# Kernel tuning notes

Measured on AMD Instinct MI355X. Metric: run time of the kernel, lower is better.

The kernel has to match this reference:

```python
import jax, jax.numpy as jnp
import numpy as np
import math

B, T, M, C, H = 4, 1024, 256, 512, 8
HD = C // H
NEG = -1e30


def setup_inputs() -> dict:
    key = jax.random.key(0)
    ks = jax.random.split(key, 16)
    s = 1.0 / math.sqrt(C)
    inp = {
        'x': jax.random.normal(ks[0], (B, T, C), jnp.float32),
        'y': jax.random.normal(ks[1], (B, M, C), jnp.float32),
        'attn_x_mask': jnp.tril(jnp.ones((T, T), bool))[None, None],  # causal (1,1,T,T)
        'Wqkv_x': jax.random.normal(ks[2], (C, 3 * C), jnp.float32) * s,
        'bqkv_x': jnp.zeros((3 * C,), jnp.float32),
        'Wqkv_y': jax.random.normal(ks[3], (C, 3 * C), jnp.float32) * s,
        'bqkv_y': jnp.zeros((3 * C,), jnp.float32),
        'w4x': jax.random.normal(ks[4], (H, HD), jnp.float32) * math.sqrt(1.0 / C / 3),
        'w4y': jax.random.normal(ks[5], (H, HD), jnp.float32) * math.sqrt(1.0 / C / 3),
        'w4xy': jax.random.normal(ks[6], (H, HD), jnp.float32) * math.sqrt(1.0 / C / 3),
        'Wgs': jax.random.normal(ks[7], (C, C), jnp.float32) * s,
        'bgs': jnp.zeros((C,), jnp.float32),
        'Wgc': jax.random.normal(ks[8], (C, C), jnp.float32) * s,
        'bgc': jnp.zeros((C,), jnp.float32),
        'Wp': jax.random.normal(ks[9], (C, C), jnp.float32) * s,
        'bp': jnp.zeros((C,), jnp.float32),
    }
    return inp


def _heads(t):
    b, n, c = t.shape
    return t.reshape(b, n, H, HD).transpose(0, 2, 1, 3)  # (B,H,N,HD)


def reference(x, y, attn_x_mask, Wqkv_x, bqkv_x, Wqkv_y, bqkv_y,
              w4x, w4y, w4xy, Wgs, bgs, Wgc, bgc, Wp, bp):
    q_x, k_x, v_x = [_heads(t) for t in jnp.split(x @ Wqkv_x + bqkv_x, 3, axis=-1)]
    q_y, k_y, v_y = [_heads(t) for t in jnp.split(y @ Wqkv_y + bqkv_y, 3, axis=-1)]
    scale = 1.0 / math.sqrt(HD)

    # additive bias attention: catt1 (per query-x), catt2 (per key-y), catt3 (bilinear)
    catt1 = jnp.einsum('bhtd,hd->bht', q_x, w4x)[..., :, None]          # (B,H,T,1)
    catt2 = jnp.einsum('bhmd,hd->bhm', q_y, w4y)[:, :, None, :]          # (B,H,1,M)
    catt3 = jnp.einsum('bhtd,bhmd->bhtm', q_x * w4xy[None, :, None, :], k_y) * scale
    catt = catt1 + catt2 + catt3                                         # (B,H,T,M)

    catt_x2y = jax.nn.softmax(catt, axis=-1)
    catt_y2x = jax.nn.softmax(catt, axis=-2)

    cval_x2y = jnp.einsum('bhtm,bhmd->bhtd', catt_x2y, v_y)
    cval_x2y = cval_x2y.transpose(0, 2, 1, 3).reshape(B, T, C)

    # product-of-attentions: (T,M) @ (M,T) -> (T,T)
    chain = jnp.einsum('bhtm,bhsm->bhts', catt_x2y, catt_y2x) * (1.0 / math.sqrt(M))
    chain = jnp.where(attn_x_mask, chain, NEG)
    chain = jax.nn.softmax(chain, axis=-1)
    cval_y2x = jnp.einsum('bhts,bhsd->bhtd', chain, v_x)
    cval_y2x = cval_y2x.transpose(0, 2, 1, 3).reshape(B, T, C)

    cval = cval_x2y + cval_y2x + x

    # masked self-attention
    satt = jnp.einsum('bhtd,bhsd->bhts', q_x, k_x) * scale
    satt = jnp.where(attn_x_mask, satt, NEG)
    satt = jax.nn.softmax(satt, axis=-1)
    sval = jnp.einsum('bhts,bhsd->bhtd', satt, v_x).transpose(0, 2, 1, 3).reshape(B, T, C)

    sgate = jax.nn.sigmoid(sval @ Wgs + bgs)
    cgate = jax.nn.sigmoid(cval @ Wgc + bgc)
    out = (sgate * cval + cgate * sval) @ Wp + bp
    return out
```

## Files before the change

kernel.cpp:

```cpp
#include <hip/hip_runtime.h>
#include <hip/hip_bf16.h>

typedef __hip_bfloat16 bf16;
using f4 = __attribute__((ext_vector_type(4))) float;
using s8 = __attribute__((ext_vector_type(8))) short;
using s4 = __attribute__((ext_vector_type(4))) short;

__device__ __forceinline__ void storeOut(float* p, float v) { *p = v; }
__device__ __forceinline__ void storeOut(bf16* p, float v) { *p = __float2bfloat16(v); }
__device__ __forceinline__ short bfs(float x) { return __builtin_bit_cast(short, __float2bfloat16(x)); }

constexpr int B_ = 4, T_ = 1024, M_ = 256, C_ = 512, H_ = 8, HD_ = 64, C3_ = 1536;

#define MFMA16(a, b, c) __builtin_amdgcn_mfma_f32_16x16x32_bf16((a), (b), (c), 0, 0, 0)

__global__ __launch_bounds__(256) void prep_kernel(
    const float* __restrict__ Wqkv_x, const float* __restrict__ Wqkv_y,
    const float* __restrict__ Wgs, const float* __restrict__ Wgc, const float* __restrict__ Wp,
    const float* __restrict__ x, const float* __restrict__ y,
    bf16* __restrict__ WT_x, bf16* __restrict__ WT_y, bf16* __restrict__ WT_gs,
    bf16* __restrict__ WT_gc, bf16* __restrict__ WT_p,
    bf16* __restrict__ x_bf, bf16* __restrict__ y_bf)
{
    __shared__ float Ls[64][65];
    const int tid = threadIdx.x;
    const int bid = blockIdx.x;
    if (bid < 576) {
        const float* W; bf16* WT; int N, t;
        if (bid < 192)      { W = Wqkv_x; WT = WT_x;  N = C3_; t = bid; }
        else if (bid < 384) { W = Wqkv_y; WT = WT_y;  N = C3_; t = bid - 192; }
        else if (bid < 448) { W = Wgs;    WT = WT_gs; N = C_;  t = bid - 384; }
        else if (bid < 512) { W = Wgc;    WT = WT_gc; N = C_;  t = bid - 448; }
        else                { W = Wp;     WT = WT_p;  N = C_;  t = bid - 512; }
        const int K = C_;
        const int tw = N >> 6;
        const int n0 = (t % tw) * 64, k0 = (t / tw) * 64;
        for (int i = tid; i < 1024; i += 256) {
            int kr = i >> 4, ng = i & 15;
            float4 v = *(const float4*)&W[(size_t)(k0 + kr) * N + n0 + ng * 4];
            Ls[ng * 4 + 0][kr] = v.x; Ls[ng * 4 + 1][kr] = v.y;
            Ls[ng * 4 + 2][kr] = v.z; Ls[ng * 4 + 3][kr] = v.w;
        }
        __syncthreads();
        for (int i = tid; i < 512; i += 256) {
            int n = i >> 3, kg = i & 7;
            s8 r;
            #pragma unroll
            for (int j = 0; j < 8; ++j) r[j] = bfs(Ls[n][kg * 8 + j]);
            *(s8*)&WT[(size_t)(n0 + n) * K + k0 + kg * 8] = r;
        }
    } else if (bid < 1600) {
        int i = (bid - 576) * 2048 + tid * 8;
        s8 r;
        #pragma unroll
        for (int j = 0; j < 8; ++j) r[j] = bfs(x[i + j]);
        *(s8*)&x_bf[i] = r;
    } else {
        int i = (bid - 1600) * 2048 + tid * 8;
        s8 r;
        #pragma unroll
        for (int j = 0; j < 8; ++j) r[j] = bfs(y[i + j]);
        *(s8*)&y_bf[i] = r;
    }
}

__global__ __launch_bounds__(256) void qwcatt_kernel(
    const bf16* __restrict__ qkv_x, const bf16* __restrict__ qkv_y,
    const float* __restrict__ w4x, const float* __restrict__ w4y,
    float* __restrict__ catt1b, float* __restrict__ catt2b)
{
    int i = blockIdx.x * 256 + threadIdx.x;
    const bf16* row; const float* w; float* out; int oi;
    if (i < 32768) {
        int bh = i >> 10, t = i & 1023, b = bh >> 3, h = bh & 7;
        row = qkv_x + (size_t)(b * T_ + t) * C3_ + h * HD_;
        w = w4x + h * HD_; out = catt1b; oi = i;
    } else {
        int j = i - 32768;
        int bh = j >> 8, m = j & 255, b = bh >> 3, h = bh & 7;
        row = qkv_y + (size_t)(b * M_ + m) * C3_ + h * HD_;
        w = w4y + h * HD_; out = catt2b; oi = j;
    }
    float s = 0.f;
    #pragma unroll
    for (int d = 0; d < HD_; ++d) s = fmaf(__bfloat162float(row[d]), w[d], s);
    out[oi] = s;
}

template <typename OT>
__global__ __launch_bounds__(256) void gemm_staged_kernel(
    const bf16* __restrict__ A, const bf16* __restrict__ WT, const float* __restrict__ bias,
    OT* __restrict__ Cmat, int N, int K)
{
    __shared__ short Asb[128][72];
    __shared__ short Bsb[64][72];
    const int tid = threadIdx.x;
    const int wave = tid >> 6, lane = tid & 63;
    const int quad = lane >> 4, l16 = lane & 15;
    const int n0 = blockIdx.y * 64, m0 = blockIdx.x * 128;
    f4 acc[2][4];
    #pragma unroll
    for (int mt = 0; mt < 2; ++mt)
        #pragma unroll
        for (int nt = 0; nt < 4; ++nt) acc[mt][nt] = (f4)0.f;

    for (int k0 = 0; k0 < K; k0 += 64) {
        #pragma unroll
        for (int tl = 0; tl < 4; ++tl) {
            int g = tid + tl * 256, row = g >> 3, grp = g & 7;
            *(s8*)&Asb[row][grp * 8] = *(const s8*)&A[(size_t)(m0 + row) * K + k0 + grp * 8];
        }
        #pragma unroll
        for (int tl = 0; tl < 2; ++tl) {
            int g = tid + tl * 256, n = g >> 3, grp = g & 7;
            *(s8*)&Bsb[n][grp * 8] = *(const s8*)&WT[(size_t)(n0 + n) * K + k0 + grp * 8];
        }
        __syncthreads();
        #pragma unroll
        for (int ks = 0; ks < 2; ++ks) {
            s8 a0 = *(const s8*)&Asb[wave * 32 + l16][ks * 32 + quad * 8];
            s8 a1 = *(const s8*)&Asb[wave * 32 + 16 + l16][ks * 32 + quad * 8];
            #pragma unroll
            for (int nt = 0; nt < 4; ++nt) {
                s8 bv = *(const s8*)&Bsb[nt * 16 + l16][ks * 32 + quad * 8];
                acc[0][nt] = MFMA16(a0, bv, acc[0][nt]);
                acc[1][nt] = MFMA16(a1, bv, acc[1][nt]);
            }
        }
        __syncthreads();
    }
    #pragma unroll
    for (int mt = 0; mt < 2; ++mt)
        #pragma unroll
        for (int nt = 0; nt < 4; ++nt) {
            int col = n0 + nt * 16 + l16;
            float bb = bias[col];
            #pragma unroll
            for (int reg = 0; reg < 4; ++reg) {
                int row = m0 + wave * 32 + mt * 16 + quad * 4 + reg;
                storeOut(&Cmat[(size_t)row * N + col], acc[mt][nt][reg] + bb);
            }
        }
}

__global__ __launch_bounds__(256) void catt3r_kernel(
    const bf16* __restrict__ qkv_x, const bf16* __restrict__ qkv_y,
    const float* __restrict__ catt1, const float* __restrict__ catt2,
    const float* __restrict__ w4xy,
    bf16* __restrict__ x2y, float* __restrict__ rowsum_, float* __restrict__ psum)
{
    __shared__ float redc[4][256];
    const int tid = threadIdx.x;
    const int wave = tid >> 6, lane = tid & 63;
    const int quad = lane >> 4, l16 = lane & 15;
    const int bh = blockIdx.x, b = bh >> 3, h = bh & 7;
    const int t0 = blockIdx.y * 64;
    f4 sc[4][4];
    #pragma unroll
    for (int mt = 0; mt < 4; ++mt)
        #pragma unroll
        for (int nt = 0; nt < 4; ++nt) sc[mt][nt] = (f4)0.f;

    const bf16* ap = qkv_x + (size_t)(b * T_ + t0 + wave * 16 + l16) * C3_ + h * HD_ + quad * 8;
    s8 a0r = *(const s8*)ap;
    s8 a1r = *(const s8*)(ap + 32);
    const float* wx = w4xy + h * HD_ + quad * 8;
    s8 a0, a1;
    #pragma unroll
    for (int j = 0; j < 8; ++j) {
        a0[j] = bfs(__bfloat162float(__builtin_bit_cast(bf16, a0r[j])) * wx[j]);
        a1[j] = bfs(__bfloat162float(__builtin_bit_cast(bf16, a1r[j])) * wx[j + 32]);
    }
    const bf16* bp = qkv_y + (size_t)(b * M_ + l16) * C3_ + C_ + h * HD_ + quad * 8;
    #pragma unroll
    for (int mt = 0; mt < 4; ++mt)
        #pragma unroll
        for (int nt = 0; nt < 4; ++nt) {
            const bf16* bq = bp + (size_t)(mt * 64 + nt * 16) * C3_;
            sc[mt][nt] = MFMA16(a0, *(const s8*)bq, sc[mt][nt]);
            sc[mt][nt] = MFMA16(a1, *(const s8*)(bq + 32), sc[mt][nt]);
        }

    float c1[4];
    #pragma unroll
    for (int reg = 0; reg < 4; ++reg)
        c1[reg] = catt1[bh * T_ + t0 + wave * 16 + quad * 4 + reg];
    #pragma unroll
    for (int mt = 0; mt < 4; ++mt)
        #pragma unroll
        for (int nt = 0; nt < 4; ++nt) {
            float c2 = catt2[bh * M_ + mt * 64 + nt * 16 + l16];
            #pragma unroll
            for (int reg = 0; reg < 4; ++reg)
                sc[mt][nt][reg] = __expf(sc[mt][nt][reg] * 0.125f + c1[reg] + c2);
        }

    #pragma unroll
    for (int reg = 0; reg < 4; ++reg) {
        float rs = 0.f;
        #pragma unroll
        for (int mt = 0; mt < 4; ++mt)
            #pragma unroll
            for (int nt = 0; nt < 4; ++nt) rs += sc[mt][nt][reg];
        rs += __shfl_xor(rs, 1); rs += __shfl_xor(rs, 2);
        rs += __shfl_xor(rs, 4); rs += __shfl_xor(rs, 8);
        const int t = t0 + wave * 16 + quad * 4 + reg;
        if (l16 == 0) rowsum_[bh * T_ + t] = rs;
        const float ri = 1.f / rs;
        #pragma unroll
        for (int mt = 0; mt < 4; ++mt)
            #pragma unroll
            for (int nt = 0; nt < 4; ++nt)
                x2y[((size_t)bh * T_ + t) * M_ + mt * 64 + nt * 16 + l16] =
                    __float2bfloat16(sc[mt][nt][reg] * ri);
    }

    #pragma unroll
    for (int mt = 0; mt < 4; ++mt)
        #pragma unroll
        for (int nt = 0; nt < 4; ++nt) {
            float es = sc[mt][nt][0] + sc[mt][nt][1] + sc[mt][nt][2] + sc[mt][nt][3];
            es += __shfl_xor(es, 16);
            es += __shfl_xor(es, 32);
            if (quad == 0) redc[wave][mt * 64 + nt * 16 + l16] = es;
        }
    __syncthreads();
    psum[((size_t)bh * 16 + blockIdx.y) * M_ + tid] =
        redc[0][tid] + redc[1][tid] + redc[2][tid] + redc[3][tid];
}

__global__ __launch_bounds__(256) void colfin_vtrans_kernel(
    const float* __restrict__ psum, float* __restrict__ colinv,
    const bf16* __restrict__ qkv_x, const bf16* __restrict__ qkv_y,
    bf16* __restrict__ vTx, bf16* __restrict__ vTy)
{
    __shared__ short Ls[64][68];
    const int tid = threadIdx.x;
    int bid = blockIdx.x;
    if (bid < 32) {
        const int bh = bid, m = tid;
        float s = 0.f;
        #pragma unroll
        for (int ch = 0; ch < 16; ++ch) s += psum[(bh * 16 + ch) * M_ + m];
        colinv[bh * M_ + m] = 1.f / s;
        return;
    }
    bid -= 32;
    const bf16* qkv; bf16* vT; int Nrows, bh, t0;
    if (bid < 512) { qkv = qkv_x; vT = vTx; Nrows = T_; bh = bid >> 4; t0 = (bid & 15) * 64; }
    else { bid -= 512; qkv = qkv_y; vT = vTy; Nrows = M_; bh = bid >> 2; t0 = (bid & 3) * 64; }
    const int b = bh >> 3, h = bh & 7;
    for (int i = tid; i < 4096; i += 256) {
        int tl = i >> 6, d = i & 63;
        Ls[d][tl] = __builtin_bit_cast(short,
            qkv[(size_t)(b * Nrows + t0 + tl) * C3_ + 2 * C_ + h * HD_ + d]);
    }
    __syncthreads();
    for (int i = tid; i < 4096; i += 256) {
        int d = i >> 6, tl = i & 63;
        vT[((size_t)bh * 64 + d) * Nrows + t0 + tl] = __builtin_bit_cast(bf16, Ls[d][tl]);
    }
}

__global__ __launch_bounds__(512) void flash14_kernel(
    const bf16* __restrict__ x2y, const float* __restrict__ rowsum_,
    const float* __restrict__ colinv,
    const bf16* __restrict__ vTx, const bf16* __restrict__ vTy,
    const bf16* __restrict__ qkv_x, const float* __restrict__ x,
    bf16* __restrict__ cval_bf, bf16* __restrict__ sval_bf)
{
    __shared__ short Kc[64][264];
    __shared__ short Ksf[64][72];
    __shared__ short Vb[64][72];
    __shared__ short Ps[8][16][68];
    const int tid = threadIdx.x;
    const int wave = tid >> 6, lane = tid & 63;
    const int quad = lane >> 4, l16 = lane & 15;
    const int bh = blockIdx.x, b = bh >> 3, h = bh & 7;
    const int p = blockIdx.y;
    const int jt = (wave < 4) ? p : (15 - p);
    const int rb = jt * 64 + (wave & 3) * 16;
    const int nst = 16 - p;

    s8 qc[8], qs[2];
    {
        const bf16* qp = x2y + (size_t)(bh * T_ + rb + l16) * M_ + quad * 8;
        #pragma unroll
        for (int f = 0; f < 8; ++f) qc[f] = *(const s8*)(qp + f * 32);
        const bf16* qsp = qkv_x + (size_t)(b * T_ + rb + l16) * C3_ + h * HD_ + quad * 8;
        qs[0] = *(const s8*)qsp;
        qs[1] = *(const s8*)(qsp + 32);
    }

    f4 ocv[4];
    #pragma unroll
    for (int dt = 0; dt < 4; ++dt) ocv[dt] = (f4)0.f;
    {
        const bf16* vb = vTy + (size_t)(bh * 64 + l16) * M_ + quad * 8;
        #pragma unroll
        for (int f = 0; f < 8; ++f)
            #pragma unroll
            for (int dt = 0; dt < 4; ++dt) {
                s8 bv = *(const s8*)(vb + (size_t)dt * 16 * M_ + f * 32);
                ocv[dt] = MFMA16(qc[f], bv, ocv[dt]);
            }
    }

    #pragma unroll
    for (int f = 0; f < 8; ++f) {
        const float* cp = colinv + bh * M_ + f * 32 + quad * 8;
        s8 q = qc[f], r;
        #pragma unroll
        for (int j = 0; j < 8; ++j)
            r[j] = bfs(__bfloat162float(__builtin_bit_cast(bf16, q[j])) * cp[j]);
        qc[f] = r;
    }

    f4 oc[4], os_[4];
    float lc[4] = {0.f, 0.f, 0.f, 0.f}, ls_[4] = {0.f, 0.f, 0.f, 0.f};
    #pragma unroll
    for (int dt = 0; dt < 4; ++dt) { oc[dt] = (f4)0.f; os_[dt] = (f4)0.f; }

    #pragma unroll
    for (int tl = 0; tl < 4; ++tl) {
        int g = tid + tl * 512, row = g >> 5, grp = g & 31;
        *(s8*)&Kc[row][grp * 8] = *(const s8*)&x2y[(size_t)(bh * T_ + row) * M_ + grp * 8];
    }
    {
        int row = tid >> 3, grp = tid & 7;
        *(s8*)&Ksf[row][grp * 8] =
            *(const s8*)&qkv_x[(size_t)(b * T_ + row) * C3_ + C_ + h * HD_ + grp * 8];
        *(s8*)&Vb[row][grp * 8] = *(const s8*)&vTx[(size_t)(bh * 64 + row) * T_ + grp * 8];
    }
    __syncthreads();

    for (int st = 0; st < nst; ++st) {
        const int s0 = st * 64;
        const bool pf = (st + 1) < nst;
        s8 kcp[4], ksp, vp;
        if (pf) {
            const int sn = s0 + 64;
            #pragma unroll
            for (int tl = 0; tl < 4; ++tl) {
                int g = tid + tl * 512, row = g >> 5, grp = g & 31;
                kcp[tl] = *(const s8*)&x2y[(size_t)(bh * T_ + sn + row) * M_ + grp * 8];
            }
            int row = tid >> 3, grp = tid & 7;
            ksp = *(const s8*)&qkv_x[(size_t)(b * T_ + sn + row) * C3_ + C_ + h * HD_ + grp * 8];
            vp = *(const s8*)&vTx[(size_t)(bh * 64 + row) * T_ + sn + grp * 8];
        }
        if (st <= jt) {
            float rsS[4];
            #pragma unroll
            for (int nt = 0; nt < 4; ++nt)
                rsS[nt] = rowsum_[bh * T_ + s0 + nt * 16 + l16] * 0.0625f;
            f4 sc[4];
            #pragma unroll
            for (int nt = 0; nt < 4; ++nt) sc[nt] = (f4)0.f;
            #pragma unroll
            for (int f = 0; f < 8; ++f)
                #pragma unroll
                for (int nt = 0; nt < 4; ++nt) {
                    s8 bv = *(const s8*)&Kc[nt * 16 + l16][f * 32 + quad * 8];
                    sc[nt] = MFMA16(qc[f], bv, sc[nt]);
                }
            f4 ss[4];
            #pragma unroll
            for (int nt = 0; nt < 4; ++nt) ss[nt] = (f4)0.f;
            #pragma unroll
            for (int f = 0; f < 2; ++f)
                #pragma unroll
                for (int nt = 0; nt < 4; ++nt) {
                    s8 bv = *(const s8*)&Ksf[nt * 16 + l16][f * 32 + quad * 8];
                    ss[nt] = MFMA16(qs[f], bv, ss[nt]);
                }
            #pragma unroll
            for (int reg = 0; reg < 4; ++reg) {
                const int t_g = rb + quad * 4 + reg;
                #pragma unroll
                for (int nt = 0; nt < 4; ++nt) {
                    float pv = (s0 + nt * 16 + l16 <= t_g) ? __expf(sc[nt][reg] * rsS[nt]) : 0.f;
                    lc[reg] += pv;
                    Ps[wave][quad * 4 + reg][nt * 16 + l16] = bfs(pv);
                }
            }
            #pragma unroll
            for (int ks = 0; ks < 2; ++ks) {
                const short* pp = &Ps[wave][l16][ks * 32 + quad * 8];
                s4 alo = *(const s4*)pp;
                s4 ahi = *(const s4*)(pp + 4);
                s8 a;
                a[0] = alo[0]; a[1] = alo[1]; a[2] = alo[2]; a[3] = alo[3];
                a[4] = ahi[0]; a[5] = ahi[1]; a[6] = ahi[2]; a[7] = ahi[3];
                #pragma unroll
                for (int dt = 0; dt < 4; ++dt) {
                    s8 bv = *(const s8*)&Vb[dt * 16 + l16][ks * 32 + quad * 8];
                    oc[dt] = MFMA16(a, bv, oc[dt]);
                }
            }
            #pragma unroll
            for (int reg = 0; reg < 4; ++reg) {
                const int t_g = rb + quad * 4 + reg;
                #pragma unroll
                for (int nt = 0; nt < 4; ++nt) {
                    float pv = (s0 + nt * 16 + l16 <= t_g) ? __expf(ss[nt][reg] * 0.125f) : 0.f;
                    ls_[reg] += pv;
                    Ps[wave][quad * 4 + reg][nt * 16 + l16] = bfs(pv);
                }
            }
            #pragma unroll
            for (int ks = 0; ks < 2; ++ks) {
                const short* pp = &Ps[wave][l16][ks * 32 + quad * 8];
                s4 alo = *(const s4*)pp;
                s4 ahi = *(const s4*)(pp + 4);
                s8 a;
                a[0] = alo[0]; a[1] = alo[1]; a[2] = alo[2]; a[3] = alo[3];
                a[4] = ahi[0]; a[5] = ahi[1]; a[6] = ahi[2]; a[7] = ahi[3];
                #pragma unroll
                for (int dt = 0; dt < 4; ++dt) {
                    s8 bv = *(const s8*)&Vb[dt * 16 + l16][ks * 32 + quad * 8];
                    os_[dt] = MFMA16(a, bv, os_[dt]);
                }
            }
        }
        __syncthreads();
        if (pf) {
            #pragma unroll
            for (int tl = 0; tl < 4; ++tl) {
                int g = tid + tl * 512, row = g >> 5, grp = g & 31;
                *(s8*)&Kc[row][grp * 8] = kcp[tl];
            }
            int row = tid >> 3, grp = tid & 7;
            *(s8*)&Ksf[row][grp * 8] = ksp;
            *(s8*)&Vb[row][grp * 8] = vp;
        }
        __syncthreads();
    }

    #pragma unroll
    for (int reg = 0; reg < 4; ++reg) {
        float l1 = lc[reg], l2 = ls_[reg];
        l1 += __shfl_xor(l1, 1); l1 += __shfl_xor(l1, 2);
        l1 += __shfl_xor(l1, 4); l1 += __shfl_xor(l1, 8);
        l2 += __shfl_xor(l2, 1); l2 += __shfl_xor(l2, 2);
        l2 += __shfl_xor(l2, 4); l2 += __shfl_xor(l2, 8);
        const float i1 = 1.f / l1, i2 = 1.f / l2;
        const int t = rb + quad * 4 + reg;
        #pragma unroll
        for (int dt = 0; dt < 4; ++dt) {
            size_t idx = (size_t)(b * T_ + t) * C_ + h * HD_ + dt * 16 + l16;
            float cv = ocv[dt][reg] + oc[dt][reg] * i1 + x[idx];
            cval_bf[idx] = __float2bfloat16(cv);
            float sv = os_[dt][reg] * i2;
            sval_bf[idx] = __float2bfloat16(sv);
        }
    }
}

__global__ __launch_bounds__(256) void gatefuse_kernel(
    const bf16* __restrict__ svalb, const bf16* __restrict__ cvalb,
    const bf16* __restrict__ WTgs, const bf16* __restrict__ WTgc,
    const float* __restrict__ bgs, const float* __restrict__ bgc,
    bf16* __restrict__ gated)
{
    __shared__ short Sb[128][72], Cb[128][72], W1b[64][72], W2b[64][72];
    const int tid = threadIdx.x;
    const int wave = tid >> 6, lane = tid & 63;
    const int quad = lane >> 4, l16 = lane & 15;
    const int n0 = blockIdx.y * 64, m0 = blockIdx.x * 128;
    f4 aS[2][4], aC[2][4];
    #pragma unroll
    for (int mt = 0; mt < 2; ++mt)
        #pragma unroll
        for (int nt = 0; nt < 4; ++nt) { aS[mt][nt] = (f4)0.f; aC[mt][nt] = (f4)0.f; }

    for (int k0 = 0; k0 < C_; k0 += 64) {
        #pragma unroll
        for (int tl = 0; tl < 4; ++tl) {
            int g = tid + tl * 256, row = g >> 3, grp = g & 7;
            *(s8*)&Sb[row][grp * 8] = *(const s8*)&svalb[(size_t)(m0 + row) * C_ + k0 + grp * 8];
            *(s8*)&Cb[row][grp * 8] = *(const s8*)&cvalb[(size_t)(m0 + row) * C_ + k0 + grp * 8];
        }
        #pragma unroll
        for (int tl = 0; tl < 2; ++tl) {
            int g = tid + tl * 256, n = g >> 3, grp = g & 7;
            *(s8*)&W1b[n][grp * 8] = *(const s8*)&WTgs[(size_t)(n0 + n) * C_ + k0 + grp * 8];
            *(s8*)&W2b[n][grp * 8] = *(const s8*)&WTgc[(size_t)(n0 + n) * C_ + k0 + grp * 8];
        }
        __syncthreads();
        #pragma unroll
        for (int ks = 0; ks < 2; ++ks) {
            s8 s0f = *(const s8*)&Sb[wave * 32 + l16][ks * 32 + quad * 8];
            s8 s1f = *(const s8*)&Sb[wave * 32 + 16 + l16][ks * 32 + quad * 8];
            s8 c0f = *(const s8*)&Cb[wave * 32 + l16][ks * 32 + quad * 8];
            s8 c1f = *(const s8*)&Cb[wave * 32 + 16 + l16][ks * 32 + quad * 8];
            #pragma unroll
            for (int nt = 0; nt < 4; ++nt) {
                s8 w1 = *(const s8*)&W1b[nt * 16 + l16][ks * 32 + quad * 8];
                s8 w2 = *(const s8*)&W2b[nt * 16 + l16][ks * 32 + quad * 8];
                aS[0][nt] = MFMA16(s0f, w1, aS[0][nt]);
                aS[1][nt] = MFMA16(s1f, w1, aS[1][nt]);
                aC[0][nt] = MFMA16(c0f, w2, aC[0][nt]);
                aC[1][nt] = MFMA16(c1f, w2, aC[1][nt]);
            }
        }
        __syncthreads();
    }
    #pragma unroll
    for (int mt = 0; mt < 2; ++mt)
        #pragma unroll
        for (int nt = 0; nt < 4; ++nt) {
            int col = n0 + nt * 16 + l16;
            float b1 = bgs[col], b2 = bgc[col];
            #pragma unroll
            for (int reg = 0; reg < 4; ++reg) {
                int row = m0 + wave * 32 + mt * 16 + quad * 4 + reg;
                size_t idx = (size_t)row * C_ + col;
                float gs = 1.f / (1.f + __expf(-(aS[mt][nt][reg] + b1)));
                float gc = 1.f / (1.f + __expf(-(aC[mt][nt][reg] + b2)));
                float cvv = __bfloat162float(cvalb[idx]);
                float svv = __bfloat162float(svalb[idx]);
                gated[idx] = __float2bfloat16(gs * cvv + gc * svv);
            }
        }
}

extern "C" void kernel_launch(void* const* d_in, const int* in_sizes, int n_in,
                              void* d_out, int out_size, void* d_ws, size_t ws_size,
                              hipStream_t stream)
{
    const float* x      = (const float*)d_in[0];
    const float* y      = (const float*)d_in[1];
    const float* Wqkv_x = (const float*)d_in[3];
    const float* bqkv_x = (const float*)d_in[4];
    const float* Wqkv_y = (const float*)d_in[5];
    const float* bqkv_y = (const float*)d_in[6];
    const float* w4x    = (const float*)d_in[7];
    const float* w4y    = (const float*)d_in[8];
    const float* w4xy   = (const float*)d_in[9];
    const float* Wgs    = (const float*)d_in[10];
    const float* bgs    = (const float*)d_in[11];
    const float* Wgc    = (const float*)d_in[12];
    const float* bgc    = (const float*)d_in[13];
    const float* Wp     = (const float*)d_in[14];
    const float* bp     = (const float*)d_in[15];

    float* ws = (float*)d_ws;
    bf16*  qkv_x_bf = (bf16*)(ws + 0);
    bf16*  qkv_y_bf = (bf16*)(ws + 3145728);
    bf16*  gated_bf = (bf16*)(ws + 3932160);
    bf16*  cval_bf  = (bf16*)(ws + 5242880);
    bf16*  x2y_bf   = (bf16*)(ws + 12320768);
    bf16*  x_bf     = x2y_bf;
    bf16*  y_bf     = (bf16*)(ws + 13369344);
    bf16*  vTx_bf   = (bf16*)(ws + 20709376);
    bf16*  vTy_bf   = (bf16*)(ws + 21757952);
    float* psum_    = ws + 22020096;
    bf16*  qw_bf    = (bf16*)(ws + 26214400);
    bf16*  sval_bf  = qw_bf;
    bf16*  WT_x     = (bf16*)(ws + 27262976);
    bf16*  WT_y     = (bf16*)(ws + 27656192);
    bf16*  WT_gs    = (bf16*)(ws + 28049408);
    bf16*  WT_gc    = (bf16*)(ws + 28180480);
    bf16*  WT_p    = (bf16*)(ws + 28311552);
    float* catt1b   = ws + 28442624;
    float* catt2b   = ws + 28475392;
    float* colinv   = ws + 28483584;
    float* rowsum_  = ws + 28491776;

    prep_kernel<<<1856, 256, 0, stream>>>(
        Wqkv_x, Wqkv_y, Wgs, Wgc, Wp, x, y,
        WT_x, WT_y, WT_gs, WT_gc, WT_p, x_bf, y_bf);

    gemm_staged_kernel<bf16><<<dim3(32, 24), 256, 0, stream>>>(x_bf, WT_x, bqkv_x, qkv_x_bf, C3_, C_);
    gemm_staged_kernel<bf16><<<dim3(8, 24), 256, 0, stream>>>(y_bf, WT_y, bqkv_y, qkv_y_bf, C3_, C_);

    qwcatt_kernel<<<160, 256, 0, stream>>>(
        qkv_x_bf, qkv_y_bf, w4x, w4y, catt1b, catt2b);

    catt3r_kernel<<<dim3(32, 16), 256, 0, stream>>>(
        qkv_x_bf, qkv_y_bf, catt1b, catt2b, w4xy, x2y_bf, rowsum_, psum_);

    colfin_vtrans_kernel<<<672, 256, 0, stream>>>(psum_, colinv, qkv_x_bf, qkv_y_bf, vTx_bf, vTy_bf);

    flash14_kernel<<<dim3(32, 8), 512, 0, stream>>>(
        x2y_bf, rowsum_, colinv, vTx_bf, vTy_bf, qkv_x_bf, x, cval_bf, sval_bf);

    gatefuse_kernel<<<dim3(32, 8), 256, 0, stream>>>(
        sval_bf, cval_bf, WT_gs, WT_gc, bgs, bgc, gated_bf);

    gemm_staged_kernel<float><<<dim3(32, 8), 256, 0, stream>>>(
        gated_bf, WT_p, bp, (float*)d_out, C_, C_);
}
```

Measured before the change: 218.9 us.

## Merge QKV GEMMs, fuse catt1/2 with V transpose, fold column finalize into flash

The x and y QKV projections now run as one launch, with the block index selecting the operand set. The catt1/catt2 dot products are merged with the V-transpose kernel. The column-sum finalization (reciprocal of the summed partials) moves into the flash kernel, which reduces psum into shared memory, so the colfin step and its colinv buffer are gone. This cuts the pipeline from several small launches to fewer and removes their launch and tail overhead. In exchange, every flash block redundantly reads 16 partial sums per column.

```diff
diff --git a/kernel.cpp b/kernel.cpp
--- a/kernel.cpp
+++ b/kernel.cpp
@@ -64,27 +64,58 @@
     }
 }
 
-__global__ __launch_bounds__(256) void qwcatt_kernel(
-    const bf16* __restrict__ qkv_x, const bf16* __restrict__ qkv_y,
-    const float* __restrict__ w4x, const float* __restrict__ w4y,
-    float* __restrict__ catt1b, float* __restrict__ catt2b)
-{
-    int i = blockIdx.x * 256 + threadIdx.x;
-    const bf16* row; const float* w; float* out; int oi;
-    if (i < 32768) {
-        int bh = i >> 10, t = i & 1023, b = bh >> 3, h = bh & 7;
-        row = qkv_x + (size_t)(b * T_ + t) * C3_ + h * HD_;
-        w = w4x + h * HD_; out = catt1b; oi = i;
-    } else {
-        int j = i - 32768;
-        int bh = j >> 8, m = j & 255, b = bh >> 3, h = bh & 7;
-        row = qkv_y + (size_t)(b * M_ + m) * C3_ + h * HD_;
-        w = w4y + h * HD_; out = catt2b; oi = j;
-    }
-    float s = 0.f;
-    #pragma unroll
-    for (int d = 0; d < HD_; ++d) s = fmaf(__bfloat162float(row[d]), w[d], s);
-    out[oi] = s;
+template <typename OT>
+__device__ __forceinline__ void gemm_body(
+    short (&Asb)[128][72], short (&Bsb)[64][72],
+    const bf16* __restrict__ A, const bf16* __restrict__ WT, const float* __restrict__ bias,
+    OT* __restrict__ Cmat, int N, int K, int m0, int n0)
+{
+    const int tid = threadIdx.x;
+    const int wave = tid >> 6, lane = tid & 63;
+    const int quad = lane >> 4, l16 = lane & 15;
+    f4 acc[2][4];
+    #pragma unroll
+    for (int mt = 0; mt < 2; ++mt)
+        #pragma unroll
+        for (int nt = 0; nt < 4; ++nt) acc[mt][nt] = (f4)0.f;
+
+    for (int k0 = 0; k0 < K; k0 += 64) {
+        #pragma unroll
+        for (int tl = 0; tl < 4; ++tl) {
+            int g = tid + tl * 256, row = g >> 3, grp = g & 7;
+            *(s8*)&Asb[row][grp * 8] = *(const s8*)&A[(size_t)(m0 + row) * K + k0 + grp * 8];
+        }
+        #pragma unroll
+        for (int tl = 0; tl < 2; ++tl) {
+            int g = tid + tl * 256, n = g >> 3, grp = g & 7;
+            *(s8*)&Bsb[n][grp * 8] = *(const s8*)&WT[(size_t)(n0 + n) * K + k0 + grp * 8];
+        }
+        __syncthreads();
+        #pragma unroll
+        for (int ks = 0; ks < 2; ++ks) {
+            s8 a0 = *(const s8*)&Asb[wave * 32 + l16][ks * 32 + quad * 8];
+            s8 a1 = *(const s8*)&Asb[wave * 32 + 16 + l16][ks * 32 + quad * 8];
+            #pragma unroll
+            for (int nt = 0; nt < 4; ++nt) {
+                s8 bv = *(const s8*)&Bsb[nt * 16 + l16][ks * 32 + quad * 8];
+                acc[0][nt] = MFMA16(a0, bv, acc[0][nt]);
+                acc[1][nt] = MFMA16(a1, bv, acc[1][nt]);
+            }
+        }
+        __syncthreads();
+    }
+    #pragma unroll
+    for (int mt = 0; mt < 2; ++mt)
+        #pragma unroll
+        for (int nt = 0; nt < 4; ++nt) {
+            int col = n0 + nt * 16 + l16;
+            float bb = bias[col];
+            #pragma unroll
+            for (int reg = 0; reg < 4; ++reg) {
+                int row = m0 + wave * 32 + mt * 16 + quad * 4 + reg;
+                storeOut(&Cmat[(size_t)row * N + col], acc[mt][nt][reg] + bb);
+            }
+        }
 }
 
 template <typename OT>
@@ -94,158 +125,55 @@
 {
     __shared__ short Asb[128][72];
     __shared__ short Bsb[64][72];
-    const int tid = threadIdx.x;
-    const int wave = tid >> 6, lane = tid & 63;
-    const int quad = lane >> 4, l16 = lane & 15;
-    const int n0 = blockIdx.y * 64, m0 = blockIdx.x * 128;
-    f4 acc[2][4];
-    #pragma unroll
-    for (int mt = 0; mt < 2; ++mt)
-        #pragma unroll
-        for (int nt = 0; nt < 4; ++nt) acc[mt][nt] = (f4)0.f;
-
-    for (int k0 = 0; k0 < K; k0 += 64) {
-        #pragma unroll
-        for (int tl = 0; tl < 4; ++tl) {
-            int g = tid + tl * 256, row = g >> 3, grp = g & 7;
-            *(s8*)&Asb[row][grp * 8] = *(const s8*)&A[(size_t)(m0 + row) * K + k0 + grp * 8];
-        }
-        #pragma unroll
-        for (int tl = 0; tl < 2; ++tl) {
-            int g = tid + tl * 256, n = g >> 3, grp = g & 7;
-            *(s8*)&Bsb[n][grp * 8] = *(const s8*)&WT[(size_t)(n0 + n) * K + k0 + grp * 8];
-        }
-        __syncthreads();
-        #pragma unroll
-        for (int ks = 0; ks < 2; ++ks) {
-            s8 a0 = *(const s8*)&Asb[wave * 32 + l16][ks * 32 + quad * 8];
-            s8 a1 = *(const s8*)&Asb[wave * 32 + 16 + l16][ks * 32 + quad * 8];
-            #pragma unroll
-            for (int nt = 0; nt < 4; ++nt) {
-                s8 bv = *(const s8*)&Bsb[nt * 16 + l16][ks * 32 + quad * 8];
-                acc[0][nt] = MFMA16(a0, bv, acc[0][nt]);
-                acc[1][nt] = MFMA16(a1, bv, acc[1][nt]);
-            }
-        }
-        __syncthreads();
-    }
-    #pragma unroll
-    for (int mt = 0; mt < 2; ++mt)
-        #pragma unroll
-        for (int nt = 0; nt < 4; ++nt) {
-            int col = n0 + nt * 16 + l16;
-            float bb = bias[col];
-            #pragma unroll
-            for (int reg = 0; reg < 4; ++reg) {
-                int row = m0 + wave * 32 + mt * 16 + quad * 4 + reg;
-                storeOut(&Cmat[(size_t)row * N + col], acc[mt][nt][reg] + bb);
-            }
-        }
-}
-
-__global__ __launch_bounds__(256) void catt3r_kernel(
+    gemm_body<OT>(Asb, Bsb, A, WT, bias, Cmat, N, K, blockIdx.x * 128, blockIdx.y * 64);
+}
+
+__global__ __launch_bounds__(256) void qkv_gemm_kernel(
+    const bf16* __restrict__ x_bf, const bf16* __restrict__ y_bf,
+    const bf16* __restrict__ WTx, const bf16* __restrict__ WTy,
+    const float* __restrict__ bqx, const float* __restrict__ bqy,
+    bf16* __restrict__ qkv_x, bf16* __restrict__ qkv_y)
+{
+    __shared__ short Asb[128][72];
+    __shared__ short Bsb[64][72];
+    const int t = blockIdx.x;
+    if (t < 768) {
+        gemm_body<bf16>(Asb, Bsb, x_bf, WTx, bqx, qkv_x, C3_, C_, (t & 31) * 128, (t >> 5) * 64);
+    } else {
+        const int u = t - 768;
+        gemm_body<bf16>(Asb, Bsb, y_bf, WTy, bqy, qkv_y, C3_, C_, (u & 7) * 128, (u >> 3) * 64);
+    }
+}
+
+__global__ __launch_bounds__(256) void catt12_vtrans_kernel(
     const bf16* __restrict__ qkv_x, const bf16* __restrict__ qkv_y,
-    const float* __restrict__ catt1, const float* __restrict__ catt2,
-    const float* __restrict__ w4xy,
-    bf16* __restrict__ x2y, float* __restrict__ rowsum_, float* __restrict__ psum)
-{
-    __shared__ float redc[4][256];
-    const int tid = threadIdx.x;
-    const int wave = tid >> 6, lane = tid & 63;
-    const int quad = lane >> 4, l16 = lane & 15;
-    const int bh = blockIdx.x, b = bh >> 3, h = bh & 7;
-    const int t0 = blockIdx.y * 64;
-    f4 sc[4][4];
-    #pragma unroll
-    for (int mt = 0; mt < 4; ++mt)
-        #pragma unroll
-        for (int nt = 0; nt < 4; ++nt) sc[mt][nt] = (f4)0.f;
-
-    const bf16* ap = qkv_x + (size_t)(b * T_ + t0 + wave * 16 + l16) * C3_ + h * HD_ + quad * 8;
-    s8 a0r = *(const s8*)ap;
-    s8 a1r = *(const s8*)(ap + 32);
-    const float* wx = w4xy + h * HD_ + quad * 8;
-    s8 a0, a1;
-    #pragma unroll
-    for (int j = 0; j < 8; ++j) {
-        a0[j] = bfs(__bfloat162float(__builtin_bit_cast(bf16, a0r[j])) * wx[j]);
-        a1[j] = bfs(__bfloat162float(__builtin_bit_cast(bf16, a1r[j])) * wx[j + 32]);
-    }
-    const bf16* bp = qkv_y + (size_t)(b * M_ + l16) * C3_ + C_ + h * HD_ + quad * 8;
-    #pragma unroll
-    for (int mt = 0; mt < 4; ++mt)
-        #pragma unroll
-        for (int nt = 0; nt < 4; ++nt) {
-            const bf16* bq = bp + (size_t)(mt * 64 + nt * 16) * C3_;
-            sc[mt][nt] = MFMA16(a0, *(const s8*)bq, sc[mt][nt]);
-            sc[mt][nt] = MFMA16(a1, *(const s8*)(bq + 32), sc[mt][nt]);
-        }
-
-    float c1[4];
-    #pragma unroll
-    for (int reg = 0; reg < 4; ++reg)
-        c1[reg] = catt1[bh * T_ + t0 + wave * 16 + quad * 4 + reg];
-    #pragma unroll
-    for (int mt = 0; mt < 4; ++mt)
-        #pragma unroll
-        for (int nt = 0; nt < 4; ++nt) {
-            float c2 = catt2[bh * M_ + mt * 64 + nt * 16 + l16];
-            #pragma unroll
-            for (int reg = 0; reg < 4; ++reg)
-                sc[mt][nt][reg] = __expf(sc[mt][nt][reg] * 0.125f + c1[reg] + c2);
-        }
-
-    #pragma unroll
-    for (int reg = 0; reg < 4; ++reg) {
-        float rs = 0.f;
-        #pragma unroll
-        for (int mt = 0; mt < 4; ++mt)
-            #pragma unroll
-            for (int nt = 0; nt < 4; ++nt) rs += sc[mt][nt][reg];
-        rs += __shfl_xor(rs, 1); rs += __shfl_xor(rs, 2);
-        rs += __shfl_xor(rs, 4); rs += __shfl_xor(rs, 8);
-        const int t = t0 + wave * 16 + quad * 4 + reg;
-        if (l16 == 0) rowsum_[bh * T_ + t] = rs;
-        const float ri = 1.f / rs;
-        #pragma unroll
-        for (int mt = 0; mt < 4; ++mt)
-            #pragma unroll
-            for (int nt = 0; nt < 4; ++nt)
-                x2y[((size_t)bh * T_ + t) * M_ + mt * 64 + nt * 16 + l16] =
-                    __float2bfloat16(sc[mt][nt][reg] * ri);
-    }
-
-    #pragma unroll
-    for (int mt = 0; mt < 4; ++mt)
-        #pragma unroll
-        for (int nt = 0; nt < 4; ++nt) {
-            float es = sc[mt][nt][0] + sc[mt][nt][1] + sc[mt][nt][2] + sc[mt][nt][3];
-            es += __shfl_xor(es, 16);
-            es += __shfl_xor(es, 32);
-            if (quad == 0) redc[wave][mt * 64 + nt * 16 + l16] = es;
-        }
-    __syncthreads();
-    psum[((size_t)bh * 16 + blockIdx.y) * M_ + tid] =
-        redc[0][tid] + redc[1][tid] + redc[2][tid] + redc[3][tid];
-}
-
-__global__ __launch_bounds__(256) void colfin_vtrans_kernel(
-    const float* __restrict__ psum, float* __restrict__ colinv,
-    const bf16* __restrict__ qkv_x, const bf16* __restrict__ qkv_y,
+    const float* __restrict__ w4x, const float* __restrict__ w4y,
+    float* __restrict__ catt1b, float* __restrict__ catt2b,
     bf16* __restrict__ vTx, bf16* __restrict__ vTy)
 {
     __shared__ short Ls[64][68];
     const int tid = threadIdx.x;
     int bid = blockIdx.x;
-    if (bid < 32) {
-        const int bh = bid, m = tid;
+    if (bid < 160) {
+        int i = bid * 256 + tid;
+        const bf16* row; const float* w; float* out; int oi;
+        if (i < 32768) {
+            int bh = i >> 10, t = i & 1023, b = bh >> 3, h = bh & 7;
+            row = qkv_x + (size_t)(b * T_ + t) * C3_ + h * HD_;
+            w = w4x + h * HD_; out = catt1b; oi = i;
+        } else {
+            int j = i - 32768;
+            int bh = j >> 8, m = j & 255, b = bh >> 3, h = bh & 7;
+            row = qkv_y + (size_t)(b * M_ + m) * C3_ + h * HD_;
+            w = w4y + h * HD_; out = catt2b; oi = j;
+        }
         float s = 0.f;
         #pragma unroll
-        for (int ch = 0; ch < 16; ++ch) s += psum[(bh * 16 + ch) * M_ + m];
-        colinv[bh * M_ + m] = 1.f / s;
+        for (int d = 0; d < HD_; ++d) s = fmaf(__bfloat162float(row[d]), w[d], s);
+        out[oi] = s;
         return;
     }
-    bid -= 32;
+    bid -= 160;
     const bf16* qkv; bf16* vT; int Nrows, bh, t0;
     if (bid < 512) { qkv = qkv_x; vT = vTx; Nrows = T_; bh = bid >> 4; t0 = (bid & 15) * 64; }
     else { bid -= 512; qkv = qkv_y; vT = vTy; Nrows = M_; bh = bid >> 2; t0 = (bid & 3) * 64; }
@@ -262,9 +190,95 @@
     }
 }
 
-__global__ __launch_bounds__(512) void flash14_kernel(
+__global__ __launch_bounds__(256) void catt3r_kernel(
+    const bf16* __restrict__ qkv_x, const bf16* __restrict__ qkv_y,
+    const float* __restrict__ catt1, const float* __restrict__ catt2,
+    const float* __restrict__ w4xy,
+    bf16* __restrict__ x2y, float* __restrict__ rowsum_, float* __restrict__ psum)
+{
+    __shared__ float redc[4][256];
+    const int tid = threadIdx.x;
+    const int wave = tid >> 6, lane = tid & 63;
+    const int quad = lane >> 4, l16 = lane & 15;
+    const int bh = blockIdx.x, b = bh >> 3, h = bh & 7;
+    const int t0 = blockIdx.y * 64;
+    f4 sc[4][4];
+    #pragma unroll
+    for (int mt = 0; mt < 4; ++mt)
+        #pragma unroll
+        for (int nt = 0; nt < 4; ++nt) sc[mt][nt] = (f4)0.f;
+
+    const bf16* ap = qkv_x + (size_t)(b * T_ + t0 + wave * 16 + l16) * C3_ + h * HD_ + quad * 8;
+    s8 a0r = *(const s8*)ap;
+    s8 a1r = *(const s8*)(ap + 32);
+    const float* wx = w4xy + h * HD_ + quad * 8;
+    s8 a0, a1;
+    #pragma unroll
+    for (int j = 0; j < 8; ++j) {
+        a0[j] = bfs(__bfloat162float(__builtin_bit_cast(bf16, a0r[j])) * wx[j]);
+        a1[j] = bfs(__bfloat162float(__builtin_bit_cast(bf16, a1r[j])) * wx[j + 32]);
+    }
+    const bf16* bp = qkv_y + (size_t)(b * M_ + l16) * C3_ + C_ + h * HD_ + quad * 8;
+    #pragma unroll
+    for (int mt = 0; mt < 4; ++mt)
+        #pragma unroll
+        for (int nt = 0; nt < 4; ++nt) {
+            const bf16* bq = bp + (size_t)(mt * 64 + nt * 16) * C3_;
+            sc[mt][nt] = MFMA16(a0, *(const s8*)bq, sc[mt][nt]);
+            sc[mt][nt] = MFMA16(a1, *(const s8*)(bq + 32), sc[mt][nt]);
+        }
+
+    float c1[4];
+    #pragma unroll
+    for (int reg = 0; reg < 4; ++reg)
+        c1[reg] = catt1[bh * T_ + t0 + wave * 16 + quad * 4 + reg];
+    #pragma unroll
+    for (int mt = 0; mt < 4; ++mt)
+        #pragma unroll
+        for (int nt = 0; nt < 4; ++nt) {
+            float c2 = catt2[bh * M_ + mt * 64 + nt * 16 + l16];
+            #pragma unroll
+            for (int reg = 0; reg < 4; ++reg)
+                sc[mt][nt][reg] = __expf(sc[mt][nt][reg] * 0.125f + c1[reg] + c2);
+        }
+
+    #pragma unroll
+    for (int reg = 0; reg < 4; ++reg) {
+        float rs = 0.f;
+        #pragma unroll
+        for (int mt = 0; mt < 4; ++mt)
+            #pragma unroll
+            for (int nt = 0; nt < 4; ++nt) rs += sc[mt][nt][reg];
+        rs += __shfl_xor(rs, 1); rs += __shfl_xor(rs, 2);
+        rs += __shfl_xor(rs, 4); rs += __shfl_xor(rs, 8);
+        const int t = t0 + wave * 16 + quad * 4 + reg;
+        if (l16 == 0) rowsum_[bh * T_ + t] = rs;
+        const float ri = 1.f / rs;
+        #pragma unroll
+        for (int mt = 0; mt < 4; ++mt)
+            #pragma unroll
+            for (int nt = 0; nt < 4; ++nt)
+                x2y[((size_t)bh * T_ + t) * M_ + mt * 64 + nt * 16 + l16] =
+                    __float2bfloat16(sc[mt][nt][reg] * ri);
+    }
+
+    #pragma unroll
+    for (int mt = 0; mt < 4; ++mt)
+        #pragma unroll
+        for (int nt = 0; nt < 4; ++nt) {
+            float es = sc[mt][nt][0] + sc[mt][nt][1] + sc[mt][nt][2] + sc[mt][nt][3];
+            es += __shfl_xor(es, 16);
+            es += __shfl_xor(es, 32);
+            if (quad == 0) redc[wave][mt * 64 + nt * 16 + l16] = es;
+        }
+    __syncthreads();
+    psum[((size_t)bh * 16 + blockIdx.y) * M_ + tid] =
+        redc[0][tid] + redc[1][tid] + redc[2][tid] + redc[3][tid];
+}
+
+__global__ __launch_bounds__(512) void flash15_kernel(
     const bf16* __restrict__ x2y, const float* __restrict__ rowsum_,
-    const float* __restrict__ colinv,
+    const float* __restrict__ psum_,
     const bf16* __restrict__ vTx, const bf16* __restrict__ vTy,
     const bf16* __restrict__ qkv_x, const float* __restrict__ x,
     bf16* __restrict__ cval_bf, bf16* __restrict__ sval_bf)
@@ -273,6 +287,7 @@
     __shared__ short Ksf[64][72];
     __shared__ short Vb[64][72];
     __shared__ short Ps[8][16][68];
+    __shared__ float cinv[256];
     const int tid = threadIdx.x;
     const int wave = tid >> 6, lane = tid & 63;
     const int quad = lane >> 4, l16 = lane & 15;
@@ -282,6 +297,13 @@
     const int rb = jt * 64 + (wave & 3) * 16;
     const int nst = 16 - p;
 
+    if (tid < 256) {
+        float s = 0.f;
+        #pragma unroll
+        for (int ch = 0; ch < 16; ++ch) s += psum_[(size_t)(bh * 16 + ch) * M_ + tid];
+        cinv[tid] = 1.f / s;
+    }
+
     s8 qc[8], qs[2];
     {
         const bf16* qp = x2y + (size_t)(bh * T_ + rb + l16) * M_ + quad * 8;
@@ -291,35 +313,6 @@
         qs[0] = *(const s8*)qsp;
         qs[1] = *(const s8*)(qsp + 32);
     }
-
-    f4 ocv[4];
-    #pragma unroll
-    for (int dt = 0; dt < 4; ++dt) ocv[dt] = (f4)0.f;
-    {
-        const bf16* vb = vTy + (size_t)(bh * 64 + l16) * M_ + quad * 8;
-        #pragma unroll
-        for (int f = 0; f < 8; ++f)
-            #pragma unroll
-            for (int dt = 0; dt < 4; ++dt) {
-                s8 bv = *(const s8*)(vb + (size_t)dt * 16 * M_ + f * 32);
-                ocv[dt] = MFMA16(qc[f], bv, ocv[dt]);
-            }
-    }
-
-    #pragma unroll
-    for (int f = 0; f < 8; ++f) {
-        const float* cp = colinv + bh * M_ + f * 32 + quad * 8;
-        s8 q = qc[f], r;
-        #pragma unroll
-        for (int j = 0; j < 8; ++j)
-            r[j] = bfs(__bfloat162float(__builtin_bit_cast(bf16, q[j])) * cp[j]);
-        qc[f] = r;
-    }
-
-    f4 oc[4], os_[4];
-    float lc[4] = {0.f, 0.f, 0.f, 0.f}, ls_[4] = {0.f, 0.f, 0.f, 0.f};
-    #pragma unroll
-    for (int dt = 0; dt < 4; ++dt) { oc[dt] = (f4)0.f; os_[dt] = (f4)0.f; }
 
     #pragma unroll
     for (int tl = 0; tl < 4; ++tl) {
@@ -333,6 +326,35 @@
         *(s8*)&Vb[row][grp * 8] = *(const s8*)&vTx[(size_t)(bh * 64 + row) * T_ + grp * 8];
     }
     __syncthreads();
+
+    f4 ocv[4];
+    #pragma unroll
+    for (int dt = 0; dt < 4; ++dt) ocv[dt] = (f4)0.f;
+    {
+        const bf16* vb = vTy + (size_t)(bh * 64 + l16) * M_ + quad * 8;
+        #pragma unroll
+        for (int f = 0; f < 8; ++f)
+            #pragma unroll
+            for (int dt = 0; dt < 4; ++dt) {
+                s8 bv = *(const s8*)(vb + (size_t)dt * 16 * M_ + f * 32);
+                ocv[dt] = MFMA16(qc[f], bv, ocv[dt]);
+            }
+    }
+
+    #pragma unroll
+    for (int f = 0; f < 8; ++f) {
+        const float* cp = &cinv[f * 32 + quad * 8];
+        s8 q = qc[f], r;
+        #pragma unroll
+        for (int j = 0; j < 8; ++j)
+            r[j] = bfs(__bfloat162float(__builtin_bit_cast(bf16, q[j])) * cp[j]);
+        qc[f] = r;
+    }
+
+    f4 oc[4], os_[4];
+    float lc[4] = {0.f, 0.f, 0.f, 0.f}, ls_[4] = {0.f, 0.f, 0.f, 0.f};
+    #pragma unroll
+    for (int dt = 0; dt < 4; ++dt) { oc[dt] = (f4)0.f; os_[dt] = (f4)0.f; }
 
     for (int st = 0; st < nst; ++st) {
         const int s0 = st * 64;
@@ -565,26 +587,23 @@
     bf16*  WT_p    = (bf16*)(ws + 28311552);
     float* catt1b   = ws + 28442624;
     float* catt2b   = ws + 28475392;
-    float* colinv   = ws + 28483584;
     float* rowsum_  = ws + 28491776;
 
     prep_kernel<<<1856, 256, 0, stream>>>(
         Wqkv_x, Wqkv_y, Wgs, Wgc, Wp, x, y,
         WT_x, WT_y, WT_gs, WT_gc, WT_p, x_bf, y_bf);
 
-    gemm_staged_kernel<bf16><<<dim3(32, 24), 256, 0, stream>>>(x_bf, WT_x, bqkv_x, qkv_x_bf, C3_, C_);
-    gemm_staged_kernel<bf16><<<dim3(8, 24), 256, 0, stream>>>(y_bf, WT_y, bqkv_y, qkv_y_bf, C3_, C_);
-
-    qwcatt_kernel<<<160, 256, 0, stream>>>(
-        qkv_x_bf, qkv_y_bf, w4x, w4y, catt1b, catt2b);
+    qkv_gemm_kernel<<<960, 256, 0, stream>>>(
+        x_bf, y_bf, WT_x, WT_y, bqkv_x, bqkv_y, qkv_x_bf, qkv_y_bf);
+
+    catt12_vtrans_kernel<<<800, 256, 0, stream>>>(
+        qkv_x_bf, qkv_y_bf, w4x, w4y, catt1b, catt2b, vTx_bf, vTy_bf);
 
     catt3r_kernel<<<dim3(32, 16), 256, 0, stream>>>(
         qkv_x_bf, qkv_y_bf, catt1b, catt2b, w4xy, x2y_bf, rowsum_, psum_);
 
-    colfin_vtrans_kernel<<<672, 256, 0, stream>>>(psum_, colinv, qkv_x_bf, qkv_y_bf, vTx_bf, vTy_bf);
-
-    flash14_kernel<<<dim3(32, 8), 512, 0, stream>>>(
-        x2y_bf, rowsum_, colinv, vTx_bf, vTy_bf, qkv_x_bf, x, cval_bf, sval_bf);
+    flash15_kernel<<<dim3(32, 8), 512, 0, stream>>>(
+        x2y_bf, rowsum_, psum_, vTx_bf, vTy_bf, qkv_x_bf, x, cval_bf, sval_bf);
 
     gatefuse_kernel<<<dim3(32, 8), 256, 0, stream>>>(
         sval_bf, cval_bf, WT_gs, WT_gc, bgs, bgc, gated_bf);
```

Measured after the change: 209.5 us. 1.04x faster.
